# Kernel tuning notes

Measured on AMD Instinct MI355X. Metric: run time of the kernel, lower is better.

Reference implementation:

```python
import jax, jax.numpy as jnp
import numpy as np

P = 0.8
XINT_MAX = 0.125; ROT_MAX = 10.0
BRI_STD = 0.2; CON_STD = 0.2; HUE_MAX = 0.95; SAT_STD = 0.2; SHARP_STD = 1.0; NOISE_STD = 0.1

def _gate(key, B, p):
    k1, k2 = jax.random.split(key)
    bern = jax.random.randint(k1, (B,), 0, 2).astype(jnp.float32)
    u = jax.random.uniform(k2, ())
    return bern * p > u  # [B] bool, matches randint(0,2)*flag*p > random()

def _sel(m, new, old):
    return jnp.where(m[:, None, None, None], new, old)

def _warp(imgs, angle_deg, tx, ty, nearest=False):
    # inverse-affine resample: rotate by angle (deg, CCW) about center, then translate (tx,ty) px; zero fill
    B, C, H, W = imgs.shape
    th = jnp.deg2rad(jnp.asarray(angle_deg, jnp.float32))
    c, s = jnp.cos(th), jnp.sin(th)
    cy, cx = (H - 1) / 2.0, (W - 1) / 2.0
    ys, xs = jnp.meshgrid(jnp.arange(H, dtype=jnp.float32), jnp.arange(W, dtype=jnp.float32), indexing='ij')
    dx = xs - cx - tx; dy = ys - cy - ty
    sx = c * dx + s * dy + cx
    sy = -s * dx + c * dy + cy
    if nearest:
        xi = jnp.round(sx); yi = jnp.round(sy)
        valid = (xi >= 0) & (xi < W) & (yi >= 0) & (yi < H)
        xc = jnp.clip(xi, 0, W - 1).astype(jnp.int32)
        yc = jnp.clip(yi, 0, H - 1).astype(jnp.int32)
        return imgs[:, :, yc, xc] * valid
    x0 = jnp.floor(sx); y0 = jnp.floor(sy)
    wx = sx - x0; wy = sy - y0
    def g(yi, xi):
        valid = (xi >= 0) & (xi < W) & (yi >= 0) & (yi < H)
        yc = jnp.clip(yi, 0, H - 1).astype(jnp.int32)
        xc = jnp.clip(xi, 0, W - 1).astype(jnp.int32)
        return imgs[:, :, yc, xc] * valid
    v00 = g(y0, x0); v01 = g(y0, x0 + 1); v10 = g(y0 + 1, x0); v11 = g(y0 + 1, x0 + 1)
    top = v00 * (1 - wx) + v01 * wx
    bot = v10 * (1 - wx) + v11 * wx
    return top * (1 - wy) + bot * wy

def _gray(x):
    return 0.2989 * x[:, 0:1] + 0.587 * x[:, 1:2] + 0.114 * x[:, 2:3]

def _blend(a, b, ratio):
    return jnp.clip(ratio * a + (1.0 - ratio) * b, 0.0, 1.0)

def _rgb_to_hsv(x):
    r, g, b = x[:, 0], x[:, 1], x[:, 2]
    maxc = jnp.maximum(jnp.maximum(r, g), b)
    minc = jnp.minimum(jnp.minimum(r, g), b)
    cr = maxc - minc
    s = cr / jnp.where(maxc == 0, 1.0, maxc)
    crd = jnp.where(cr == 0, 1.0, cr)
    rc = (maxc - r) / crd; gc = (maxc - g) / crd; bc = (maxc - b) / crd
    h = jnp.where(maxc == r, bc - gc, jnp.where(maxc == g, 2.0 + rc - bc, 4.0 + gc - rc))
    h = jnp.where(cr == 0, 0.0, (h / 6.0) % 1.0)
    return jnp.stack([h, s, maxc], axis=1)

def _hsv_to_rgb(x):
    h, s, v = x[:, 0], x[:, 1], x[:, 2]
    i = jnp.floor(h * 6.0)
    f = h * 6.0 - i
    p = v * (1 - s); q = v * (1 - f * s); t = v * (1 - (1 - f) * s)
    ii = i.astype(jnp.int32) % 6
    conds = [ii == 0, ii == 1, ii == 2, ii == 3, ii == 4, ii == 5]
    r = jnp.select(conds, [v, q, p, p, t, v])
    g = jnp.select(conds, [t, v, v, q, p, p])
    b = jnp.select(conds, [p, p, t, v, v, q])
    return jnp.stack([r, g, b], axis=1)

def _sharp_degenerate(x):
    C, H, W = x.shape[1], x.shape[2], x.shape[3]
    k = jnp.array([[1., 1., 1.], [1., 5., 1.], [1., 1., 1.]], jnp.float32) / 13.0
    w = jnp.tile(k[None, None], (C, 1, 1, 1))
    blur = jax.lax.conv_general_dilated(x, w, (1, 1), 'SAME', feature_group_count=C,
                                        dimension_numbers=('NCHW', 'OIHW', 'NCHW'))
    blur = jnp.clip(blur, 0.0, 1.0)
    interior = jnp.zeros((H, W), bool).at[1:-1, 1:-1].set(True)
    return jnp.where(interior, blur, x)  # torchvision keeps original border pixels

def _augment(images, masks):
    key = jax.random.key(42)
    ks = jax.random.split(key, 18)
    B = images.shape[0]
    img = (images + 1.0) * 0.5
    msk = masks
    # xflip
    m = _gate(ks[0], B, P)
    img = _sel(m, img[:, :, :, ::-1], img)
    msk = _sel(m, msk[:, :, :, ::-1], msk)
    # rotate90 (square images: exact)
    m = _gate(ks[1], B, P)
    img = _sel(m, jnp.rot90(img, 1, axes=(2, 3)), img)
    msk = _sel(m, jnp.rot90(msk, 1, axes=(2, 3)), msk)
    # xint translation
    m = _gate(ks[2], B, P)
    t = jax.random.uniform(ks[3], ()) * XINT_MAX
    img = _sel(m, _warp(img, 0.0, t, t), img)
    msk = _sel(m, _warp(msk, 0.0, t, t, nearest=True), msk)
    # rotate
    m = _gate(ks[4], B, P)
    r = jax.random.uniform(ks[5], ()) * ROT_MAX
    img = _sel(m, _warp(img, r, 0.0, 0.0), img)
    msk = _sel(m, _warp(msk, r, 0.0, 0.0, nearest=True), msk)
    # hue
    m = _gate(ks[6], B, P)
    h = (jax.random.uniform(ks[7], ()) - 0.5) * HUE_MAX
    hsv = _rgb_to_hsv(jnp.clip(img, 0.0, 1.0))
    hsv = hsv.at[:, 0].set((hsv[:, 0] + h) % 1.0)
    img = _sel(m, _hsv_to_rgb(hsv), img)
    # brightness
    m = _gate(ks[8], B, P)
    b = jnp.abs(1.0 + jax.random.normal(ks[9], ()) * BRI_STD)
    img = _sel(m, jnp.clip(img * b, 0.0, 1.0), img)
    # contrast
    m = _gate(ks[10], B, P)
    c = jnp.abs(1.0 + jax.random.normal(ks[11], ()) * CON_STD)
    mean = _gray(img).mean(axis=(2, 3), keepdims=True)
    img = _sel(m, _blend(img, mean, c), img)
    # saturation
    m = _gate(ks[12], B, P)
    s = jnp.abs(1.0 + jax.random.normal(ks[13], ()) * SAT_STD)
    img = _sel(m, _blend(img, _gray(img), s), img)
    # sharpness (bug-faithful: std == self.sharpness == 1.0)
    m = _gate(ks[14], B, P)
    sh = jnp.abs(1.0 + jax.random.normal(ks[15], ()) * SHARP_STD)
    img = _sel(m, _blend(img, _sharp_degenerate(img), sh), img)
    # noise
    m = _gate(ks[16], B, P)
    n = jax.random.normal(ks[17], img.shape, img.dtype) * NOISE_STD
    img = _sel(m, img + n, img)
    img = (img - 0.5) / 0.5
    return img, msk

def setup_inputs() -> dict:
    key = jax.random.key(0)
    k1, k2 = jax.random.split(key)
    images = jax.random.uniform(k1, (32, 3, 512, 512), jnp.float32, -1.0, 1.0)
    masks = (jax.random.uniform(k2, (32, 1, 512, 512), jnp.float32) > 0.5).astype(jnp.float32)
    return {"images": images, "masks": masks}

def reference(images, masks):
    return _augment(images, masks)
```

## Files before the change

kernel.cpp:

```cpp
#include <hip/hip_runtime.h>
#include <stdint.h>
#include <math.h>

#define HH 512
#define WW 512
#define BB 32
#define CC 3
#define HWSZ (HH*WW)
#define CHW (CC*HWSZ)
#define NIMG (BB*CHW)
#define NMSK (BB*HWSZ)

__host__ __device__ inline uint32_t rotl32(uint32_t x, uint32_t r){ return (x<<r)|(x>>(32u-r)); }

__host__ __device__ inline void tf2x32(uint32_t k0, uint32_t k1, uint32_t x0, uint32_t x1,
                                       uint32_t& o0, uint32_t& o1){
  uint32_t kx = k0 ^ k1 ^ 0x1BD11BDAu;
  uint32_t ks[3] = {k0, k1, kx};
  const uint32_t R[2][4] = {{13u,15u,26u,6u},{17u,29u,16u,24u}};
  x0 += ks[0]; x1 += ks[1];
  #pragma unroll
  for (int i = 0; i < 5; ++i){
    #pragma unroll
    for (int j = 0; j < 4; ++j){
      x0 += x1; x1 = rotl32(x1, R[i & 1][j]); x1 ^= x0;
    }
    x0 += ks[(i+1)%3];
    x1 += ks[(i+2)%3] + (uint32_t)(i+1);
  }
  o0 = x0; o1 = x1;
}

__host__ __device__ inline float bits_to_u01(uint32_t b){
  uint32_t fb = (b >> 9) | 0x3f800000u;
  float f;
#ifdef __HIP_DEVICE_COMPILE__
  f = __uint_as_float(fb);
#else
  union { uint32_t u; float f; } cv; cv.u = fb; f = cv.f;
#endif
  return f - 1.0f;
}

__host__ __device__ inline float erfinv_f32(float x){
  float w = -log1pf(-x*x);
  float p;
  if (w < 5.0f){
    w -= 2.5f;
    p = 2.81022636e-08f;
    p = fmaf(p, w, 3.43273939e-07f);
    p = fmaf(p, w, -3.5233877e-06f);
    p = fmaf(p, w, -4.39150654e-06f);
    p = fmaf(p, w, 0.00021858087f);
    p = fmaf(p, w, -0.00125372503f);
    p = fmaf(p, w, -0.00417768164f);
    p = fmaf(p, w, 0.246640727f);
    p = fmaf(p, w, 1.50140941f);
  } else {
    w = sqrtf(w) - 3.0f;
    p = -0.000200214257f;
    p = fmaf(p, w, 0.000100950558f);
    p = fmaf(p, w, 0.00134934322f);
    p = fmaf(p, w, -0.00367342844f);
    p = fmaf(p, w, 0.00573950773f);
    p = fmaf(p, w, -0.0076224613f);
    p = fmaf(p, w, 0.00943887047f);
    p = fmaf(p, w, 1.00167406f);
    p = fmaf(p, w, 2.83297682f);
  }
  return p * x;
}

#define NRM_LO (-0.9999999403953552f)
#define SQRT2F 1.41421356237309504880f

__host__ __device__ inline float normal_from_bits(uint32_t b){
  float f = bits_to_u01(b);
  float val = f * 2.0f + NRM_LO;
  val = fmaxf(NRM_LO, val);
  return SQRT2F * erfinv_f32(val);
}

struct Key { uint32_t a, b; };

static Key foldSplit(Key k, uint32_t j){
  Key r; tf2x32(k.a, k.b, 0u, j, r.a, r.b); return r;
}

static uint32_t bits32(Key k, uint32_t i){
  uint32_t o0, o1; tf2x32(k.a, k.b, 0u, i, o0, o1); return o0 ^ o1;
}

static float unif_scalar(Key k){ return bits_to_u01(bits32(k, 0u)); }
static float normal_scalar(Key k){ return normal_from_bits(bits32(k, 0u)); }

static uint32_t gate_mask(Key kg){
  Key k1 = foldSplit(kg, 0u);
  Key k2 = foldSplit(kg, 1u);
  Key kl = foldSplit(k1, 1u);
  float u = bits_to_u01(bits32(k2, 0u));
  uint32_t m = 0;
  for (uint32_t i = 0; i < 32; ++i){
    float bern = (float)(bits32(kl, i) & 1u);
    if (bern * 0.8f > u) m |= (1u << i);
  }
  return m;
}

struct AugParams {
  uint32_t mFlip, mRot90, mTrans, mRot, mHue, mBri, mCon, mSat, mSharp, mNoise;
  float t, rotC, rotS, hShift, bri, con, sat, shp;
  uint32_t nk0, nk1;
};

__device__ inline float clip01(float v){ return fminf(fmaxf(v, 0.0f), 1.0f); }

__device__ inline void permIdx(int y, int x, bool r9, bool fl, int& py, int& px){
  if (r9){ py = x; px = 511 - y; } else { py = y; px = x; }
  if (fl) px = 511 - px;
}

__device__ inline float tapP(const float* __restrict__ src, int y, int x, bool r9, bool fl){
  if ((unsigned)x >= 512u || (unsigned)y >= 512u) return 0.0f;
  int py, px; permIdx(y, x, r9, fl, py, px);
  return (src[py*512 + px] + 1.0f) * 0.5f;
}

__device__ inline void stage1RGB(const float* __restrict__ base, int ty, int tx,
                                 bool r9, bool fl, bool tr, float t, float out[3]){
  if (!tr){
    #pragma unroll
    for (int c = 0; c < 3; ++c) out[c] = tapP(base + c*HWSZ, ty, tx, r9, fl);
    return;
  }
  float sx = (((float)tx - 255.5f) - t) + 255.5f;
  float sy = (((float)ty - 255.5f) - t) + 255.5f;
  float x0f = floorf(sx), y0f = floorf(sy);
  float wx = sx - x0f, wy = sy - y0f;
  int x0 = (int)x0f, y0 = (int)y0f;
  #pragma unroll
  for (int c = 0; c < 3; ++c){
    const float* s = base + c*HWSZ;
    float v00 = tapP(s, y0,   x0,   r9, fl);
    float v01 = tapP(s, y0,   x0+1, r9, fl);
    float v10 = tapP(s, y0+1, x0,   r9, fl);
    float v11 = tapP(s, y0+1, x0+1, r9, fl);
    float top = v00*(1.0f-wx) + v01*wx;
    float bot = v10*(1.0f-wx) + v11*wx;
    out[c] = top*(1.0f-wy) + bot*wy;
  }
}

__device__ inline void rotTap(const float* __restrict__ base, int ty, int tx,
                              bool r9, bool fl, bool tr, float t, float o[3]){
  if ((unsigned)tx < 512u && (unsigned)ty < 512u){
    stage1RGB(base, ty, tx, r9, fl, tr, t, o);
  } else {
    o[0] = o[1] = o[2] = 0.0f;
  }
}

__device__ inline void rgb2hsv(float r, float g, float b, float& h, float& s, float& v){
  float maxc = fmaxf(fmaxf(r, g), b);
  float minc = fminf(fminf(r, g), b);
  float cr = maxc - minc;
  s = cr / ((maxc == 0.0f) ? 1.0f : maxc);
  float crd = (cr == 0.0f) ? 1.0f : cr;
  float rc = (maxc - r) / crd;
  float gc = (maxc - g) / crd;
  float bc = (maxc - b) / crd;
  float hh = (maxc == r) ? (bc - gc) : ((maxc == g) ? (2.0f + rc - bc) : (4.0f + gc - rc));
  float hd = hh / 6.0f;
  hd = hd - floorf(hd);
  h = (cr == 0.0f) ? 0.0f : hd;
  v = maxc;
}

__device__ inline void hsv2rgb(float h, float s, float v, float& r, float& g, float& b){
  float i = floorf(h * 6.0f);
  float f = h * 6.0f - i;
  float p = v * (1.0f - s);
  float q = v * (1.0f - f * s);
  float t = v * (1.0f - (1.0f - f) * s);
  int ii = ((int)i) % 6;
  r = (ii == 0 || ii == 5) ? v : (ii == 1) ? q : (ii == 4) ? t : p;
  g = (ii == 0) ? t : (ii <= 2) ? v : (ii == 3) ? q : p;
  b = (ii <= 1) ? p : (ii == 2) ? t : (ii <= 4) ? v : q;
}

__device__ inline void applyHB(float v[3], bool hue, bool bri, const AugParams& P){
  if (hue){
    float r = clip01(v[0]), g = clip01(v[1]), bb = clip01(v[2]);
    float h, s, val;
    rgb2hsv(r, g, bb, h, s, val);
    h = h + P.hShift;
    h = h - floorf(h);
    hsv2rgb(h, s, val, v[0], v[1], v[2]);
  }
  if (bri){
    #pragma unroll
    for (int c = 0; c < 3; ++c) v[c] = clip01(v[c] * P.bri);
  }
}

__device__ inline void stage2RGB(const float* __restrict__ base, int yy, int xx,
                                 const AugParams& P, int b, float v[3]){
  bool fl  = (P.mFlip  >> b) & 1u;
  bool r9  = (P.mRot90 >> b) & 1u;
  bool tr  = (P.mTrans >> b) & 1u;
  bool rot = (P.mRot   >> b) & 1u;
  if (rot){
    float dx = (float)xx - 255.5f;
    float dy = (float)yy - 255.5f;
    float sx = (P.rotC*dx + P.rotS*dy) + 255.5f;
    float sy = (-P.rotS*dx + P.rotC*dy) + 255.5f;
    float x0f = floorf(sx), y0f = floorf(sy);
    float wx = sx - x0f, wy = sy - y0f;
    int x0 = (int)x0f, y0 = (int)y0f;
    float q00[3], q01[3], q10[3], q11[3];
    rotTap(base, y0,   x0,   r9, fl, tr, P.t, q00);
    rotTap(base, y0,   x0+1, r9, fl, tr, P.t, q01);
    rotTap(base, y0+1, x0,   r9, fl, tr, P.t, q10);
    rotTap(base, y0+1, x0+1, r9, fl, tr, P.t, q11);
    #pragma unroll
    for (int c = 0; c < 3; ++c){
      float top = q00[c]*(1.0f-wx) + q01[c]*wx;
      float bot = q10[c]*(1.0f-wx) + q11[c]*wx;
      v[c] = top*(1.0f-wy) + bot*wy;
    }
  } else {
    stage1RGB(base, yy, xx, r9, fl, tr, P.t, v);
  }
  applyHB(v, (P.mHue >> b) & 1u, (P.mBri >> b) & 1u, P);
}

__device__ inline float s1at(const float* __restrict__ s, int y, int x){
  return ((unsigned)x < 512u && (unsigned)y < 512u) ? s[y*512 + x] : 0.0f;
}

__device__ inline void stage2S1(const float* __restrict__ s1b, int yy, int xx,
                                const AugParams& P, int b, float v[3]){
  bool rot = (P.mRot >> b) & 1u;
  bool hue = (P.mHue >> b) & 1u;
  bool bri = (P.mBri >> b) & 1u;
  if (rot){
    float dx = (float)xx - 255.5f;
    float dy = (float)yy - 255.5f;
    float sx = (P.rotC*dx + P.rotS*dy) + 255.5f;
    float sy = (-P.rotS*dx + P.rotC*dy) + 255.5f;
    float x0f = floorf(sx), y0f = floorf(sy);
    float wx = sx - x0f, wy = sy - y0f;
    int x0 = (int)x0f, y0 = (int)y0f;
    #pragma unroll
    for (int c = 0; c < 3; ++c){
      const float* s = s1b + c*HWSZ;
      float v00 = s1at(s, y0,   x0);
      float v01 = s1at(s, y0,   x0+1);
      float v10 = s1at(s, y0+1, x0);
      float v11 = s1at(s, y0+1, x0+1);
      float top = v00*(1.0f-wx) + v01*wx;
      float bot = v10*(1.0f-wx) + v11*wx;
      v[c] = top*(1.0f-wy) + bot*wy;
    }
  } else {
    #pragma unroll
    for (int c = 0; c < 3; ++c) v[c] = s1b[c*HWSZ + yy*512 + xx];
  }
  applyHB(v, hue, bri, P);
}

__device__ inline void procCS(float v[3], bool con, float cmul, float cadd, bool sat, float smul){
  if (con){
    #pragma unroll
    for (int c = 0; c < 3; ++c) v[c] = clip01(cmul * v[c] + cadd);
  }
  if (sat){
    float g = 0.2989f*v[0] + 0.587f*v[1] + 0.114f*v[2];
    float gadd = (1.0f - smul) * g;
    #pragma unroll
    for (int c = 0; c < 3; ++c) v[c] = clip01(smul * v[c] + gadd);
  }
}



__global__ __launch_bounds__(256) void kStage1M(const float* __restrict__ img,
                                                const float* __restrict__ msk,
                                                float* __restrict__ S1,
                                                float* __restrict__ M1,
                                                float* __restrict__ outMsk,
                                                float* __restrict__ meanAcc, AugParams P){
  __shared__ float ptile[3][33][33];
  __shared__ float wsum[4];
  int zz = blockIdx.z;
  int tx = threadIdx.x, ty = threadIdx.y;
  int tid = ty*32 + tx;
  int X0 = blockIdx.x*32, Y0 = blockIdx.y*32;

  if (zz >= BB){
    int b = zz - BB;
    bool fl  = (P.mFlip  >> b) & 1u;
    bool r9  = (P.mRot90 >> b) & 1u;
    bool rot = (P.mRot   >> b) & 1u;
    const float* src = msk + (size_t)b*HWSZ;
    float* dst = (rot ? M1 : outMsk) + (size_t)b*HWSZ;
    if (!r9){
      int row = tid >> 3, q = tid & 7;
      int y = Y0 + row, x4 = X0 + q*4;
      float4 u;
      if (!fl){
        u = *(const float4*)(src + y*512 + x4);
      } else {
        float4 w = *(const float4*)(src + y*512 + (508 - x4));
        u = make_float4(w.w, w.z, w.y, w.x);
      }
      *(float4*)(dst + y*512 + x4) = u;
    } else {
      float (*mtile)[33] = reinterpret_cast<float(*)[33]>(&ptile[0][0][0]);
      for (int idx = tid; idx < 32*32; idx += 256){
        int r = idx >> 5, q = idx & 31;
        int xx = X0 + r;
        int yy = Y0 + q;
        int col = fl ? yy : (511 - yy);
        mtile[q][r] = src[xx*512 + col];
      }
      __syncthreads();
      #pragma unroll
      for (int k = 0; k < 4; ++k){
        int y = Y0 + ty + 8*k, x = X0 + tx;
        dst[y*512 + x] = mtile[ty + 8*k][tx];
      }
    }
    return;
  }

  int b = zz;
  bool fl  = (P.mFlip  >> b) & 1u;
  bool r9  = (P.mRot90 >> b) & 1u;
  bool tr  = (P.mTrans >> b) & 1u;
  bool rot = (P.mRot   >> b) & 1u;
  bool con = (P.mCon   >> b) & 1u;
  bool hue = (P.mHue   >> b) & 1u;
  bool bri = (P.mBri   >> b) & 1u;
  bool accM = con && !rot;
  const float* base = img + (size_t)b*CHW;
  float* dstb = S1 + (size_t)b*CHW;
  float t = P.t;
  float gsum = 0.0f;

  if (!r9 && !tr){
    int row = tid >> 3, q = tid & 7;
    int y = Y0 + row, x4 = X0 + q*4;
    float vv[3][4];
    #pragma unroll
    for (int c = 0; c < 3; ++c){
      float4 u;
      if (!fl){
        u = *(const float4*)(base + c*HWSZ + y*512 + x4);
      } else {
        float4 w = *(const float4*)(base + c*HWSZ + y*512 + (508 - x4));
        u = make_float4(w.w, w.z, w.y, w.x);
      }
      u.x = (u.x + 1.0f)*0.5f; u.y = (u.y + 1.0f)*0.5f;
      u.z = (u.z + 1.0f)*0.5f; u.w = (u.w + 1.0f)*0.5f;
      *(float4*)(dstb + c*HWSZ + y*512 + x4) = u;
      vv[c][0] = u.x; vv[c][1] = u.y; vv[c][2] = u.z; vv[c][3] = u.w;
    }
    if (accM){
      #pragma unroll
      for (int e = 0; e < 4; ++e){
        float w[3] = {vv[0][e], vv[1][e], vv[2][e]};
        applyHB(w, hue, bri, P);
        gsum += 0.2989f*w[0] + 0.587f*w[1] + 0.114f*w[2];
      }
    }
  } else if (!r9){
    #pragma unroll
    for (int k = 0; k < 4; ++k){
      int y = Y0 + ty + 8*k, x = X0 + tx;
      float v[3];
      stage1RGB(base, y, x, false, fl, true, t, v);
      #pragma unroll
      for (int c = 0; c < 3; ++c)
        dstb[(size_t)c*HWSZ + (size_t)y*512 + x] = v[c];
      if (accM){
        float w[3] = {v[0], v[1], v[2]};
        applyHB(w, hue, bri, P);
        gsum += 0.2989f*w[0] + 0.587f*w[1] + 0.114f*w[2];
      }
    }
  } else {
    #pragma unroll
    for (int c = 0; c < 3; ++c){
      const float* src = base + c*HWSZ;
      for (int idx = tid; idx < 33*33; idx += 256){
        int r = idx / 33, q = idx - r*33;
        int xx = X0 - 1 + r;
        int yy = Y0 - 1 + q;
        float val = 0.0f;
        if ((unsigned)yy < 512u && (unsigned)xx < 512u){
          int col = fl ? yy : (511 - yy);
          val = (src[xx*512 + col] + 1.0f) * 0.5f;
        }
        ptile[c][q][r] = val;
      }
    }
    __syncthreads();
    #pragma unroll
    for (int k = 0; k < 4; ++k){
      int y = Y0 + ty + 8*k, x = X0 + tx;
      float v[3];
      if (tr){
        float sx = (((float)x - 255.5f) - t) + 255.5f;
        float sy = (((float)y - 255.5f) - t) + 255.5f;
        float x0f = floorf(sx), y0f = floorf(sy);
        float wx = sx - x0f, wy = sy - y0f;
        int lx0 = (int)x0f - (X0 - 1);
        int ly0 = (int)y0f - (Y0 - 1);
        #pragma unroll
        for (int c = 0; c < 3; ++c){
          float v00 = ptile[c][ly0][lx0],   v01 = ptile[c][ly0][lx0+1];
          float v10 = ptile[c][ly0+1][lx0], v11 = ptile[c][ly0+1][lx0+1];
          float top = v00*(1.0f-wx) + v01*wx;
          float bot = v10*(1.0f-wx) + v11*wx;
          v[c] = top*(1.0f-wy) + bot*wy;
        }
      } else {
        #pragma unroll
        for (int c = 0; c < 3; ++c) v[c] = ptile[c][ty+8*k+1][tx+1];
      }
      #pragma unroll
      for (int c = 0; c < 3; ++c)
        dstb[(size_t)c*HWSZ + (size_t)y*512 + x] = v[c];
      if (accM){
        float w[3] = {v[0], v[1], v[2]};
        applyHB(w, hue, bri, P);
        gsum += 0.2989f*w[0] + 0.587f*w[1] + 0.114f*w[2];
      }
    }
  }

  if (accM){
    #pragma unroll
    for (int off = 32; off > 0; off >>= 1) gsum += __shfl_down(gsum, off);
    int wid = tid >> 6, lid = tid & 63;
    if (lid == 0) wsum[wid] = gsum;
    __syncthreads();
    if (tid == 0) atomicAdd(&meanAcc[b], wsum[0] + wsum[1] + wsum[2] + wsum[3]);
  }
}

__global__ __launch_bounds__(256) void kMean2(const float* __restrict__ S1,
                                              float* __restrict__ meanAcc, AugParams P){
  int b = blockIdx.z;
  if (!((P.mCon >> b) & 1u) || !((P.mRot >> b) & 1u)) return;
  int tid = threadIdx.x;
  const float* base = S1 + (size_t)b*CHW;
  int pbase = blockIdx.x * 4096;
  float lsum = 0.0f;

  #pragma unroll 4
  for (int j = 0; j < 16; ++j){
    int px = pbase + j*256 + tid;
    int y = px >> 9, x = px & 511;
    float v[3];
    stage2S1(base, y, x, P, b, v);
    lsum += 0.2989f*v[0] + 0.587f*v[1] + 0.114f*v[2];
  }

  #pragma unroll
  for (int off = 32; off > 0; off >>= 1) lsum += __shfl_down(lsum, off);
  __shared__ float wsum[4];
  int wid = tid >> 6, lid = tid & 63;
  if (lid == 0) wsum[wid] = lsum;
  __syncthreads();
  if (tid == 0) atomicAdd(&meanAcc[b], wsum[0] + wsum[1] + wsum[2] + wsum[3]);
}

__global__ __launch_bounds__(256) void kFinalM(const float* __restrict__ S1,
                                               const float* __restrict__ M1,
                                               const float* __restrict__ meanAcc,
                                               float* __restrict__ out,
                                               float* __restrict__ outMsk, AugParams P){
  __shared__ float s2[34][34][3];
  int zz = blockIdx.z;
  int tx = threadIdx.x, ty = threadIdx.y;
  int tid = ty*32 + tx;
  int bx = blockIdx.x, by = blockIdx.y;

  if (zz >= BB){
    int b = zz - BB;
    if (!((P.mRot >> b) & 1u)) return;
    const float* src = M1 + (size_t)b*HWSZ;
    float* dst = outMsk + (size_t)b*HWSZ;
    int X0 = bx*32, Y0 = by*32;
    #pragma unroll
    for (int k = 0; k < 4; ++k){
      int x = X0 + tx, y = Y0 + ty + 8*k;
      float dx = __fsub_rn((float)x, 255.5f);
      float dy = __fsub_rn((float)y, 255.5f);
      float sx = __fadd_rn(__fadd_rn(__fmul_rn(P.rotC, dx), __fmul_rn(P.rotS, dy)), 255.5f);
      float sy = __fadd_rn(__fadd_rn(__fmul_rn(-P.rotS, dx), __fmul_rn(P.rotC, dy)), 255.5f);
      float xi = rintf(sx), yi = rintf(sy);
      bool valid = (xi >= 0.0f) && (xi < 512.0f) && (yi >= 0.0f) && (yi < 512.0f);
      int xc = (int)fminf(fmaxf(xi, 0.0f), 511.0f);
      int yc = (int)fminf(fmaxf(yi, 0.0f), 511.0f);
      float v = valid ? src[yc*512 + xc] : 0.0f;
      dst[y*512 + x] = v;
    }
    return;
  }

  int b = zz;
  const float W1 = 1.0f/13.0f, W5 = 5.0f/13.0f;
  bool rot = (P.mRot   >> b) & 1u;
  bool hue = (P.mHue   >> b) & 1u;
  bool bri = (P.mBri   >> b) & 1u;
  bool con = (P.mCon   >> b) & 1u;
  bool sat = (P.mSat   >> b) & 1u;
  bool shg = (P.mSharp >> b) & 1u;
  bool noi = (P.mNoise >> b) & 1u;
  float mean = meanAcc[b] * (1.0f/262144.0f);
  float cadd = (1.0f - P.con) * mean;
  const float* base = S1 + (size_t)b*CHW;

  if (!shg && !rot){
    int row = tid >> 3, q = tid & 7;
    int y = by*32 + row; int x4 = bx*32 + q*4;
    float4 rv = *(const float4*)(base + y*512 + x4);
    float4 gv = *(const float4*)(base + HWSZ + y*512 + x4);
    float4 bv = *(const float4*)(base + 2*HWSZ + y*512 + x4);
    float R[4] = {rv.x, rv.y, rv.z, rv.w};
    float G[4] = {gv.x, gv.y, gv.z, gv.w};
    float B[4] = {bv.x, bv.y, bv.z, bv.w};
    float O[3][4];
    #pragma unroll
    for (int e = 0; e < 4; ++e){
      float v[3] = {R[e], G[e], B[e]};
      applyHB(v, hue, bri, P);
      procCS(v, con, P.con, cadd, sat, P.sat);
      if (noi){
        #pragma unroll
        for (int c = 0; c < 3; ++c){
          uint32_t idx = (uint32_t)(b*CHW + c*HWSZ + y*512 + x4 + e);
          uint32_t o0, o1;
          tf2x32(P.nk0, P.nk1, 0u, idx, o0, o1);
          v[c] += normal_from_bits(o0 ^ o1) * 0.1f;
        }
      }
      #pragma unroll
      for (int c = 0; c < 3; ++c) O[c][e] = (v[c] - 0.5f) * 2.0f;
    }
    #pragma unroll
    for (int c = 0; c < 3; ++c){
      float4 w = make_float4(O[c][0], O[c][1], O[c][2], O[c][3]);
      *(float4*)(out + (size_t)b*CHW + (size_t)c*HWSZ + (size_t)y*512 + x4) = w;
    }
    return;
  }

  if (!shg){
    #pragma unroll
    for (int k = 0; k < 4; ++k){
      int x = bx*32 + tx, y = by*32 + ty + 8*k;
      float res[3];
      stage2S1(base, y, x, P, b, res);
      procCS(res, con, P.con, cadd, sat, P.sat);
      if (noi){
        #pragma unroll
        for (int c = 0; c < 3; ++c){
          uint32_t idx = (uint32_t)(b*CHW + c*HWSZ + y*512 + x);
          uint32_t o0, o1;
          tf2x32(P.nk0, P.nk1, 0u, idx, o0, o1);
          res[c] += normal_from_bits(o0 ^ o1) * 0.1f;
        }
      }
      #pragma unroll
      for (int c = 0; c < 3; ++c){
        out[(size_t)b*CHW + (size_t)c*HWSZ + (size_t)y*512 + x] = (res[c] - 0.5f) * 2.0f;
      }
    }
    return;
  }

  for (int cell = tid; cell < 34*34; cell += 256){
    int r = cell / 34, cc = cell - r*34;
    int gy = by*32 + r - 1, gx = bx*32 + cc - 1;
    float v[3] = {0.0f, 0.0f, 0.0f};
    if ((unsigned)gx < 512u && (unsigned)gy < 512u){
      stage2S1(base, gy, gx, P, b, v);
      procCS(v, con, P.con, cadd, sat, P.sat);
    }
    s2[r][cc][0] = v[0]; s2[r][cc][1] = v[1]; s2[r][cc][2] = v[2];
  }
  __syncthreads();

  for (int k = 0; k < 4; ++k){
    int yy = ty + 8*k;
    int x = bx*32 + tx, y = by*32 + yy;
    bool interior = (x >= 1) && (x <= 510) && (y >= 1) && (y <= 510);
    float res[3];
    float c0[3] = { s2[yy+1][tx+1][0], s2[yy+1][tx+1][1], s2[yy+1][tx+1][2] };
    if (interior){
      float nsum[3] = {0.0f, 0.0f, 0.0f};
      #pragma unroll
      for (int dy = 0; dy < 3; ++dy){
        #pragma unroll
        for (int dxx = 0; dxx < 3; ++dxx){
          if (dxx == 1 && dy == 1) continue;
          #pragma unroll
          for (int c = 0; c < 3; ++c) nsum[c] += s2[yy+dy][tx+dxx][c];
        }
      }
      #pragma unroll
      for (int c = 0; c < 3; ++c){
        float bl = clip01(nsum[c]*W1 + c0[c]*W5);
        res[c] = clip01(P.shp * c0[c] + (1.0f - P.shp) * bl);
      }
    } else {
      res[0] = c0[0]; res[1] = c0[1]; res[2] = c0[2];
    }

    if (noi){
      #pragma unroll
      for (int c = 0; c < 3; ++c){
        uint32_t idx = (uint32_t)(b*CHW + c*HWSZ + y*512 + x);
        uint32_t o0, o1;
        tf2x32(P.nk0, P.nk1, 0u, idx, o0, o1);
        res[c] += normal_from_bits(o0 ^ o1) * 0.1f;
      }
    }
    #pragma unroll
    for (int c = 0; c < 3; ++c){
      out[(size_t)b*CHW + (size_t)c*HWSZ + (size_t)y*512 + x] = (res[c] - 0.5f) * 2.0f;
    }
  }
}


__global__ __launch_bounds__(256) void kMask(const float* __restrict__ msk,
                                             float* __restrict__ out, AugParams P){
  int x = blockIdx.x*blockDim.x + threadIdx.x;
  int y = blockIdx.y*blockDim.y + threadIdx.y;
  int b = blockIdx.z;
  bool fl  = (P.mFlip  >> b) & 1u;
  bool r9  = (P.mRot90 >> b) & 1u;
  bool rot = (P.mRot   >> b) & 1u;
  float v;
  if (rot){
    float dx = __fsub_rn((float)x, 255.5f);
    float dy = __fsub_rn((float)y, 255.5f);
    float sx = __fadd_rn(__fadd_rn(__fmul_rn(P.rotC, dx), __fmul_rn(P.rotS, dy)), 255.5f);
    float sy = __fadd_rn(__fadd_rn(__fmul_rn(-P.rotS, dx), __fmul_rn(P.rotC, dy)), 255.5f);
    float xi = rintf(sx), yi = rintf(sy);
    bool valid = (xi >= 0.0f) && (xi < 512.0f) && (yi >= 0.0f) && (yi < 512.0f);
    int xc = (int)fminf(fmaxf(xi, 0.0f), 511.0f);
    int yc = (int)fminf(fmaxf(yi, 0.0f), 511.0f);
    int py, px; permIdx(yc, xc, r9, fl, py, px);
    v = valid ? msk[(size_t)b*HWSZ + py*512 + px] : 0.0f;
  } else {
    int py, px; permIdx(y, x, r9, fl, py, px);
    v = msk[(size_t)b*HWSZ + py*512 + px];
  }
  out[(size_t)b*HWSZ + y*512 + x] = v;
}

__global__ __launch_bounds__(256) void kMean(const float* __restrict__ img,
                                             float* __restrict__ meanAcc, AugParams P){
  int b = blockIdx.z;
  if (!((P.mCon >> b) & 1u)) return;
  int x = blockIdx.x*blockDim.x + threadIdx.x;
  int y = blockIdx.y*blockDim.y + threadIdx.y;
  float v[3];
  stage2RGB(img + (size_t)b*CHW, y, x, P, b, v);
  float gray = 0.2989f*v[0] + 0.587f*v[1] + 0.114f*v[2];
  __shared__ float sred[256];
  int tid = threadIdx.y*blockDim.x + threadIdx.x;
  sred[tid] = gray;
  __syncthreads();
  for (int s = 128; s > 0; s >>= 1){
    if (tid < s) sred[tid] += sred[tid + s];
    __syncthreads();
  }
  if (tid == 0) atomicAdd(&meanAcc[b], sred[0]);
}

__global__ __launch_bounds__(256) void kFinal(const float* __restrict__ img,
                                              const float* __restrict__ meanAcc,
                                              float* __restrict__ out, AugParams P){
  __shared__ float s2[10][34][3];
  int tx = threadIdx.x, ty = threadIdx.y;
  int tid = ty*32 + tx;
  int bx = blockIdx.x, by = blockIdx.y, b = blockIdx.z;
  const float W1 = 1.0f/13.0f, W5 = 5.0f/13.0f;

  bool con = (P.mCon   >> b) & 1u;
  bool sat = (P.mSat   >> b) & 1u;
  bool shg = (P.mSharp >> b) & 1u;
  bool noi = (P.mNoise >> b) & 1u;
  float mean = meanAcc[b] * (1.0f/262144.0f);
  float cadd = (1.0f - P.con) * mean;
  const float* base = img + (size_t)b*CHW;

  for (int cell = tid; cell < 340; cell += 256){
    int r = cell / 34, cc = cell % 34;
    int gy = by*8 + r - 1, gx = bx*32 + cc - 1;
    float v[3] = {0.0f, 0.0f, 0.0f};
    if ((unsigned)gx < 512u && (unsigned)gy < 512u){
      stage2RGB(base, gy, gx, P, b, v);
      procCS(v, con, P.con, cadd, sat, P.sat);
    }
    s2[r][cc][0] = v[0]; s2[r][cc][1] = v[1]; s2[r][cc][2] = v[2];
  }
  __syncthreads();

  int x = bx*32 + tx, y = by*8 + ty;
  bool interior = (x >= 1) && (x <= 510) && (y >= 1) && (y <= 510);
  float res[3];
  float c0[3] = { s2[ty+1][tx+1][0], s2[ty+1][tx+1][1], s2[ty+1][tx+1][2] };
  if (shg && interior){
    float nsum[3] = {0.0f, 0.0f, 0.0f};
    #pragma unroll
    for (int dy = 0; dy < 3; ++dy){
      #pragma unroll
      for (int dxx = 0; dxx < 3; ++dxx){
        if (dxx == 1 && dy == 1) continue;
        #pragma unroll
        for (int c = 0; c < 3; ++c) nsum[c] += s2[ty+dy][tx+dxx][c];
      }
    }
    #pragma unroll
    for (int c = 0; c < 3; ++c){
      float bl = clip01(nsum[c]*W1 + c0[c]*W5);
      res[c] = clip01(P.shp * c0[c] + (1.0f - P.shp) * bl);
    }
  } else {
    res[0] = c0[0]; res[1] = c0[1]; res[2] = c0[2];
  }

  if (noi){
    #pragma unroll
    for (int c = 0; c < 3; ++c){
      uint32_t idx = (uint32_t)(b*CHW + c*HWSZ + y*512 + x);
      uint32_t o0, o1;
      tf2x32(P.nk0, P.nk1, 0u, idx, o0, o1);
      res[c] += normal_from_bits(o0 ^ o1) * 0.1f;
    }
  }
  #pragma unroll
  for (int c = 0; c < 3; ++c){
    out[(size_t)b*CHW + (size_t)c*HWSZ + y*512 + x] = (res[c] - 0.5f) * 2.0f;
  }
}

extern "C" void kernel_launch(void* const* d_in, const int* in_sizes, int n_in,
                              void* d_out, int out_size, void* d_ws, size_t ws_size,
                              hipStream_t stream) {
  (void)in_sizes; (void)n_in; (void)out_size;
  const float* images = (const float*)d_in[0];
  const float* masks  = (const float*)d_in[1];
  float* out_img = (float*)d_out;
  float* out_msk = out_img + (size_t)NIMG;
  float* meanAcc = (float*)d_ws;

  Key root; root.a = 0u; root.b = 42u;
  Key ks[18];
  for (uint32_t j = 0; j < 18; ++j) ks[j] = foldSplit(root, j);

  AugParams P;
  P.mFlip  = gate_mask(ks[0]);
  P.mRot90 = gate_mask(ks[1]);
  P.mTrans = gate_mask(ks[2]);
  P.t      = unif_scalar(ks[3]) * 0.125f;
  P.mRot   = gate_mask(ks[4]);
  float r  = unif_scalar(ks[5]) * 10.0f;
  P.mHue   = gate_mask(ks[6]);
  P.hShift = (unif_scalar(ks[7]) - 0.5f) * 0.95f;
  P.mBri   = gate_mask(ks[8]);
  P.bri    = fabsf(1.0f + normal_scalar(ks[9])  * 0.2f);
  P.mCon   = gate_mask(ks[10]);
  P.con    = fabsf(1.0f + normal_scalar(ks[11]) * 0.2f);
  P.mSat   = gate_mask(ks[12]);
  P.sat    = fabsf(1.0f + normal_scalar(ks[13]) * 0.2f);
  P.mSharp = gate_mask(ks[14]);
  P.shp    = fabsf(1.0f + normal_scalar(ks[15]) * 1.0f);
  P.mNoise = gate_mask(ks[16]);
  P.nk0 = ks[17].a; P.nk1 = ks[17].b;

  if (!(P.t > 0.0f)) P.mTrans = 0u;

  float th = r * 0.017453292519943295f;
  P.rotC = (float)cos((double)th);
  P.rotS = (float)sin((double)th);

  dim3 blk(32, 8, 1);
  const size_t needFull = ((size_t)NIMG + (size_t)NMSK + 64) * sizeof(float);
  const size_t needImg  = ((size_t)NIMG + 64) * sizeof(float);

  hipMemsetAsync(meanAcc, 0, 32*sizeof(float), stream);

  if (ws_size >= needFull){
    float* S1 = (float*)d_ws + 64;
    float* M1 = S1 + (size_t)NIMG;
    kStage1M<<<dim3(16, 16, 64), blk, 0, stream>>>(images, masks, S1, M1, out_msk, meanAcc, P);
    kMean2  <<<dim3(64, 1, 32), dim3(256,1,1), 0, stream>>>(S1, meanAcc, P);
    kFinalM <<<dim3(16, 16, 64), blk, 0, stream>>>(S1, M1, meanAcc, out_img, out_msk, P);
  } else if (ws_size >= needImg){
    float* S1 = (float*)d_ws + 64;
    kMask   <<<dim3(16, 64, 32), blk, 0, stream>>>(masks, out_msk, P);
    kStage1M<<<dim3(16, 16, 32), blk, 0, stream>>>(images, masks, S1, nullptr, out_msk, meanAcc, P);
    kMean2  <<<dim3(64, 1, 32), dim3(256,1,1), 0, stream>>>(S1, meanAcc, P);
    kFinalM <<<dim3(16, 16, 32), blk, 0, stream>>>(S1, nullptr, meanAcc, out_img, out_msk, P);
  } else {
    kMask <<<dim3(16, 64, 32), blk, 0, stream>>>(masks, out_msk, P);
    kMean <<<dim3(16, 64, 32), blk, 0, stream>>>(images, meanAcc, P);
    kFinal<<<dim3(16, 64, 32), blk, 0, stream>>>(images, meanAcc, out_img, P);
  }
}
```

Before: 358.6 us.

## Skip intermediate S1 buffer for non-rotated images, recompute stage-1 in final kernel

For images without the arbitrary rotation, stage 1 no longer writes the normalized/flipped/translated image to the S1 workspace. It only computes the contrast mean when needed. The final kernel now reads the original input and recomputes flip, translate and rot90 on the fly through stage2RGB. This removes a full-image write and re-read for most images, at the cost of recomputing the geometric transforms and reading the input twice when contrast is active.

```diff
diff --git a/kernel.cpp b/kernel.cpp
--- a/kernel.cpp
+++ b/kernel.cpp
@@ -340,18 +340,32 @@
   bool tr  = (P.mTrans >> b) & 1u;
   bool rot = (P.mRot   >> b) & 1u;
   bool con = (P.mCon   >> b) & 1u;
-  bool hue = (P.mHue   >> b) & 1u;
-  bool bri = (P.mBri   >> b) & 1u;
-  bool accM = con && !rot;
   const float* base = img + (size_t)b*CHW;
+  float t = P.t;
+
+  if (!rot){
+    if (!con) return;
+    float gsum = 0.0f;
+    #pragma unroll
+    for (int k = 0; k < 4; ++k){
+      int y = Y0 + ty + 8*k, x = X0 + tx;
+      float v[3];
+      stage2RGB(base, y, x, P, b, v);
+      gsum += 0.2989f*v[0] + 0.587f*v[1] + 0.114f*v[2];
+    }
+    #pragma unroll
+    for (int off = 32; off > 0; off >>= 1) gsum += __shfl_down(gsum, off);
+    int wid = tid >> 6, lid = tid & 63;
+    if (lid == 0) wsum[wid] = gsum;
+    __syncthreads();
+    if (tid == 0) atomicAdd(&meanAcc[b], wsum[0] + wsum[1] + wsum[2] + wsum[3]);
+    return;
+  }
+
   float* dstb = S1 + (size_t)b*CHW;
-  float t = P.t;
-  float gsum = 0.0f;
-
   if (!r9 && !tr){
     int row = tid >> 3, q = tid & 7;
     int y = Y0 + row, x4 = X0 + q*4;
-    float vv[3][4];
     #pragma unroll
     for (int c = 0; c < 3; ++c){
       float4 u;
@@ -364,15 +378,6 @@
       u.x = (u.x + 1.0f)*0.5f; u.y = (u.y + 1.0f)*0.5f;
       u.z = (u.z + 1.0f)*0.5f; u.w = (u.w + 1.0f)*0.5f;
       *(float4*)(dstb + c*HWSZ + y*512 + x4) = u;
-      vv[c][0] = u.x; vv[c][1] = u.y; vv[c][2] = u.z; vv[c][3] = u.w;
-    }
-    if (accM){
-      #pragma unroll
-      for (int e = 0; e < 4; ++e){
-        float w[3] = {vv[0][e], vv[1][e], vv[2][e]};
-        applyHB(w, hue, bri, P);
-        gsum += 0.2989f*w[0] + 0.587f*w[1] + 0.114f*w[2];
-      }
     }
   } else if (!r9){
     #pragma unroll
@@ -383,11 +388,6 @@
       #pragma unroll
       for (int c = 0; c < 3; ++c)
         dstb[(size_t)c*HWSZ + (size_t)y*512 + x] = v[c];
-      if (accM){
-        float w[3] = {v[0], v[1], v[2]};
-        applyHB(w, hue, bri, P);
-        gsum += 0.2989f*w[0] + 0.587f*w[1] + 0.114f*w[2];
-      }
     }
   } else {
     #pragma unroll
@@ -432,21 +432,7 @@
       #pragma unroll
       for (int c = 0; c < 3; ++c)
         dstb[(size_t)c*HWSZ + (size_t)y*512 + x] = v[c];
-      if (accM){
-        float w[3] = {v[0], v[1], v[2]};
-        applyHB(w, hue, bri, P);
-        gsum += 0.2989f*w[0] + 0.587f*w[1] + 0.114f*w[2];
-      }
-    }
-  }
-
-  if (accM){
-    #pragma unroll
-    for (int off = 32; off > 0; off >>= 1) gsum += __shfl_down(gsum, off);
-    int wid = tid >> 6, lid = tid & 63;
-    if (lid == 0) wsum[wid] = gsum;
-    __syncthreads();
-    if (tid == 0) atomicAdd(&meanAcc[b], wsum[0] + wsum[1] + wsum[2] + wsum[3]);
+    }
   }
 }
 
@@ -477,7 +463,8 @@
   if (tid == 0) atomicAdd(&meanAcc[b], wsum[0] + wsum[1] + wsum[2] + wsum[3]);
 }
 
-__global__ __launch_bounds__(256) void kFinalM(const float* __restrict__ S1,
+__global__ __launch_bounds__(256) void kFinalM(const float* __restrict__ img,
+                                               const float* __restrict__ S1,
                                                const float* __restrict__ M1,
                                                const float* __restrict__ meanAcc,
                                                float* __restrict__ out,
@@ -513,6 +500,9 @@
 
   int b = zz;
   const float W1 = 1.0f/13.0f, W5 = 5.0f/13.0f;
+  bool fl  = (P.mFlip  >> b) & 1u;
+  bool r9  = (P.mRot90 >> b) & 1u;
+  bool tr  = (P.mTrans >> b) & 1u;
   bool rot = (P.mRot   >> b) & 1u;
   bool hue = (P.mHue   >> b) & 1u;
   bool bri = (P.mBri   >> b) & 1u;
@@ -522,21 +512,32 @@
   bool noi = (P.mNoise >> b) & 1u;
   float mean = meanAcc[b] * (1.0f/262144.0f);
   float cadd = (1.0f - P.con) * mean;
-  const float* base = S1 + (size_t)b*CHW;
-
-  if (!shg && !rot){
+  const float* s1b = S1 + (size_t)b*CHW;
+  const float* imb = img + (size_t)b*CHW;
+
+  if (!shg && !rot && !r9 && !tr){
     int row = tid >> 3, q = tid & 7;
     int y = by*32 + row; int x4 = bx*32 + q*4;
-    float4 rv = *(const float4*)(base + y*512 + x4);
-    float4 gv = *(const float4*)(base + HWSZ + y*512 + x4);
-    float4 bv = *(const float4*)(base + 2*HWSZ + y*512 + x4);
+    float4 rv, gv, bv;
+    if (!fl){
+      rv = *(const float4*)(imb + y*512 + x4);
+      gv = *(const float4*)(imb + HWSZ + y*512 + x4);
+      bv = *(const float4*)(imb + 2*HWSZ + y*512 + x4);
+    } else {
+      float4 rw = *(const float4*)(imb + y*512 + (508 - x4));
+      float4 gw = *(const float4*)(imb + HWSZ + y*512 + (508 - x4));
+      float4 bw = *(const float4*)(imb + 2*HWSZ + y*512 + (508 - x4));
+      rv = make_float4(rw.w, rw.z, rw.y, rw.x);
+      gv = make_float4(gw.w, gw.z, gw.y, gw.x);
+      bv = make_float4(bw.w, bw.z, bw.y, bw.x);
+    }
     float R[4] = {rv.x, rv.y, rv.z, rv.w};
     float G[4] = {gv.x, gv.y, gv.z, gv.w};
     float B[4] = {bv.x, bv.y, bv.z, bv.w};
     float O[3][4];
     #pragma unroll
     for (int e = 0; e < 4; ++e){
-      float v[3] = {R[e], G[e], B[e]};
+      float v[3] = {(R[e]+1.0f)*0.5f, (G[e]+1.0f)*0.5f, (B[e]+1.0f)*0.5f};
       applyHB(v, hue, bri, P);
       procCS(v, con, P.con, cadd, sat, P.sat);
       if (noi){
@@ -564,7 +565,8 @@
     for (int k = 0; k < 4; ++k){
       int x = bx*32 + tx, y = by*32 + ty + 8*k;
       float res[3];
-      stage2S1(base, y, x, P, b, res);
+      if (rot) stage2S1(s1b, y, x, P, b, res);
+      else     stage2RGB(imb, y, x, P, b, res);
       procCS(res, con, P.con, cadd, sat, P.sat);
       if (noi){
         #pragma unroll
@@ -588,7 +590,8 @@
     int gy = by*32 + r - 1, gx = bx*32 + cc - 1;
     float v[3] = {0.0f, 0.0f, 0.0f};
     if ((unsigned)gx < 512u && (unsigned)gy < 512u){
-      stage2S1(base, gy, gx, P, b, v);
+      if (rot) stage2S1(s1b, gy, gx, P, b, v);
+      else     stage2RGB(imb, gy, gx, P, b, v);
       procCS(v, con, P.con, cadd, sat, P.sat);
     }
     s2[r][cc][0] = v[0]; s2[r][cc][1] = v[1]; s2[r][cc][2] = v[2];
@@ -804,13 +807,13 @@
     float* M1 = S1 + (size_t)NIMG;
     kStage1M<<<dim3(16, 16, 64), blk, 0, stream>>>(images, masks, S1, M1, out_msk, meanAcc, P);
     kMean2  <<<dim3(64, 1, 32), dim3(256,1,1), 0, stream>>>(S1, meanAcc, P);
-    kFinalM <<<dim3(16, 16, 64), blk, 0, stream>>>(S1, M1, meanAcc, out_img, out_msk, P);
+    kFinalM <<<dim3(16, 16, 64), blk, 0, stream>>>(images, S1, M1, meanAcc, out_img, out_msk, P);
   } else if (ws_size >= needImg){
     float* S1 = (float*)d_ws + 64;
     kMask   <<<dim3(16, 64, 32), blk, 0, stream>>>(masks, out_msk, P);
     kStage1M<<<dim3(16, 16, 32), blk, 0, stream>>>(images, masks, S1, nullptr, out_msk, meanAcc, P);
     kMean2  <<<dim3(64, 1, 32), dim3(256,1,1), 0, stream>>>(S1, meanAcc, P);
-    kFinalM <<<dim3(16, 16, 32), blk, 0, stream>>>(S1, nullptr, meanAcc, out_img, out_msk, P);
+    kFinalM <<<dim3(16, 16, 32), blk, 0, stream>>>(images, S1, nullptr, meanAcc, out_img, out_msk, P);
   } else {
     kMask <<<dim3(16, 64, 32), blk, 0, stream>>>(masks, out_msk, P);
     kMean <<<dim3(16, 64, 32), blk, 0, stream>>>(images, meanAcc, P);
```

New measurement: 388.0 us. 8.2% more time.
